# Optimization experiments

Measured on AMD Instinct MI355X. Metric: run time of the kernel, lower is better.

The kernel has to match this reference:

```python
import jax, jax.numpy as jnp
import numpy as np

B, S, D, H, DF = 8, 1024, 1024, 16, 4096
DK = D // H
EPS = 1e-5


def setup_inputs() -> dict:
    key = jax.random.key(0)
    ks = jax.random.split(key, 16)
    w = lambda k, shape: (jax.random.normal(k, shape, jnp.float32) * 0.02)
    inp = {
        "x": jax.random.normal(ks[0], (B, S, D), jnp.float32),
        "mask": jnp.ones((B, 1, 1, S), jnp.int32),
        # attention projections (torch Linear: y = x @ W.T + b)
        "Wq": w(ks[1], (D, D)), "bq": jnp.zeros((D,), jnp.float32),
        "Wk": w(ks[2], (D, D)), "bk": jnp.zeros((D,), jnp.float32),
        "Wv": w(ks[3], (D, D)), "bv": jnp.zeros((D,), jnp.float32),
        "Wo": w(ks[4], (D, D)), "bo": jnp.zeros((D,), jnp.float32),
        "ln_attn_g": jnp.ones((D,), jnp.float32), "ln_attn_b": jnp.zeros((D,), jnp.float32),
        # feed-forward
        "W1": w(ks[5], (DF, D)), "b1": jnp.zeros((DF,), jnp.float32),
        "W2": w(ks[6], (D, DF)), "b2": jnp.zeros((D,), jnp.float32),
        "ln_ff_g": jnp.ones((D,), jnp.float32), "ln_ff_b": jnp.zeros((D,), jnp.float32),
        # BatchNorm1d(d_ff) inside FFN (eval mode: running stats)
        "bnff_g": jnp.ones((DF,), jnp.float32), "bnff_b": jnp.zeros((DF,), jnp.float32),
        "bnff_m": jnp.zeros((DF,), jnp.float32), "bnff_v": jnp.ones((DF,), jnp.float32),
        # BatchNorm1d(d_model) after each sublayer (eval mode)
        "bn1_g": jnp.ones((D,), jnp.float32), "bn1_b": jnp.zeros((D,), jnp.float32),
        "bn1_m": jnp.zeros((D,), jnp.float32), "bn1_v": jnp.ones((D,), jnp.float32),
        "bn2_g": jnp.ones((D,), jnp.float32), "bn2_b": jnp.zeros((D,), jnp.float32),
        "bn2_m": jnp.zeros((D,), jnp.float32), "bn2_v": jnp.ones((D,), jnp.float32),
    }
    return inp


def _layernorm(x, g, b):
    mu = jnp.mean(x, axis=-1, keepdims=True)
    var = jnp.mean(jnp.square(x - mu), axis=-1, keepdims=True)
    return (x - mu) * jax.lax.rsqrt(var + EPS) * g + b


def _batchnorm_eval(x, g, b, m, v):
    # x: [B,S,C]; BatchNorm1d over channel C (the transpose->bn->transpose in torch
    # is equivalent to per-channel affine normalization on the last dim in eval mode)
    return (x - m) * jax.lax.rsqrt(v + EPS) * g + b


def reference(x, mask, Wq, bq, Wk, bk, Wv, bv, Wo, bo, ln_attn_g, ln_attn_b,
              W1, b1, W2, b2, ln_ff_g, ln_ff_b,
              bnff_g, bnff_b, bnff_m, bnff_v,
              bn1_g, bn1_b, bn1_m, bn1_v,
              bn2_g, bn2_b, bn2_m, bn2_v):
    # ---- Multi-head self-attention (pre-LN on query/key/value input) ----
    xq = _layernorm(x, ln_attn_g, ln_attn_b)
    q = (xq @ Wq.T + bq).reshape(B, S, H, DK)
    k = (x @ Wk.T + bk).reshape(B, S, H, DK)   # note: original applies LN only to `query`;
    v = (x @ Wv.T + bv).reshape(B, S, H, DK)   # key/value are passed raw (same x here)
    scores = jnp.einsum("bqhd,bkhd->bhqk", q, k) / np.sqrt(DK).astype(np.float32)
    scores = jnp.where(mask == 0, jnp.float32(-1e9), scores)
    attn = jax.nn.softmax(scores, axis=-1)                      # [B,H,S,S]
    context = jnp.einsum("bhqk,bkhd->bqhd", attn, v).reshape(B, S, D)
    attn_out = context @ Wo.T + bo
    x = x + attn_out                                            # residual (eval: no dropout)
    x = _batchnorm_eval(x, bn1_g, bn1_b, bn1_m, bn1_v)
    # ---- Position-wise FFN ----
    xn = _layernorm(x, ln_ff_g, ln_ff_b)
    h = jax.nn.gelu(xn @ W1.T + b1, approximate=False)          # [B,S,DF]
    h = _batchnorm_eval(h, bnff_g, bnff_b, bnff_m, bnff_v)
    ff = h @ W2.T + b2
    x = x + ff
    x = _batchnorm_eval(x, bn2_g, bn2_b, bn2_m, bn2_v)
    return x, attn
```

## Files before the change

kernel.cpp:

```cpp
#include <hip/hip_runtime.h>
#include <hip/hip_bf16.h>
#include <math.h>

typedef __hip_bfloat16 bf16;
typedef __attribute__((ext_vector_type(8))) short short8;
typedef __attribute__((ext_vector_type(4))) short short4v;
typedef __attribute__((ext_vector_type(4))) float f32x4;

#define DEV static __device__ __forceinline__

DEV short f2bf(float f) {
    bf16 h = __float2bfloat16(f);
    return __builtin_bit_cast(short, h);
}

DEV void glds16(const void* g, void* l) {
    __builtin_amdgcn_global_load_lds((const __attribute__((address_space(1))) void*)g,
                                     (__attribute__((address_space(3))) void*)l, 16, 0, 0);
}

__global__ __launch_bounds__(256) void cast_all(const float* __restrict__ Wq,
                                                const float* __restrict__ Wk,
                                                const float* __restrict__ Wv,
                                                const float* __restrict__ Wo,
                                                const float* __restrict__ W1,
                                                const float* __restrict__ W2,
                                                bf16* __restrict__ wqkv, bf16* __restrict__ wo,
                                                bf16* __restrict__ w1, bf16* __restrict__ w2) {
    int i = blockIdx.x * 256 + threadIdx.x;
    const float* src;
    bf16* dst;
    int si, di;
    if (i < 786432) {
        src = (i < 262144) ? Wq : (i < 524288) ? Wk : Wv;
        si = (i < 262144) ? i : (i < 524288) ? i - 262144 : i - 524288;
        dst = wqkv; di = i;
    } else if (i < 1048576) {
        src = Wo; si = i - 786432; dst = wo; di = si;
    } else if (i < 2097152) {
        src = W1; si = i - 1048576; dst = w1; di = si;
    } else {
        src = W2; si = i - 2097152; dst = w2; di = si;
    }
    f32x4 v = ((const f32x4*)src)[si];
    short4v o;
    #pragma unroll
    for (int j = 0; j < 4; j++) o[j] = f2bf(v[j]);
    ((short4v*)dst)[di] = o;
}

__global__ __launch_bounds__(256) void affine_all(
    const float* __restrict__ g1, const float* __restrict__ bb1, const float* __restrict__ m1, const float* __restrict__ v1,
    const float* __restrict__ g2, const float* __restrict__ bb2, const float* __restrict__ m2, const float* __restrict__ v2,
    const float* __restrict__ gf, const float* __restrict__ bbf, const float* __restrict__ mf, const float* __restrict__ vf,
    float* __restrict__ s1, float* __restrict__ t1, float* __restrict__ s2, float* __restrict__ t2,
    float* __restrict__ sf, float* __restrict__ tf) {
    int i = blockIdx.x * 256 + threadIdx.x;
    const float *g, *b, *m, *v; float *s, *t; int j;
    if (i < 1024)      { g = g1; b = bb1; m = m1; v = v1; s = s1; t = t1; j = i; }
    else if (i < 2048) { g = g2; b = bb2; m = m2; v = v2; s = s2; t = t2; j = i - 1024; }
    else               { g = gf; b = bbf; m = mf; v = vf; s = sf; t = tf; j = i - 2048; }
    float sc = g[j] * rsqrtf(v[j] + 1e-5f);
    s[j] = sc;
    t[j] = b[j] - m[j] * sc;
}

__global__ __launch_bounds__(256) void ln_kernel(const float* __restrict__ x,
                                                 const float* __restrict__ g,
                                                 const float* __restrict__ b,
                                                 bf16* __restrict__ lnout,
                                                 bf16* __restrict__ rawout) {
    const int row = blockIdx.x, t = threadIdx.x;
    const float* xr = x + (size_t)row * 1024;
    f32x4 v = ((const f32x4*)xr)[t];
    float s = v[0] + v[1] + v[2] + v[3];
    float sq = v[0]*v[0] + v[1]*v[1] + v[2]*v[2] + v[3]*v[3];
    #pragma unroll
    for (int off = 1; off < 64; off <<= 1) {
        s  += __shfl_xor(s, off);
        sq += __shfl_xor(sq, off);
    }
    __shared__ float ls[4], lq[4];
    if ((t & 63) == 0) { ls[t >> 6] = s; lq[t >> 6] = sq; }
    __syncthreads();
    s = ls[0] + ls[1] + ls[2] + ls[3];
    sq = lq[0] + lq[1] + lq[2] + lq[3];
    float mu = s * (1.0f / 1024.0f);
    float rs = rsqrtf(sq * (1.0f / 1024.0f) - mu * mu + 1e-5f);
    f32x4 gg = ((const f32x4*)g)[t];
    f32x4 bb = ((const f32x4*)b)[t];
    short4v o;
    #pragma unroll
    for (int j = 0; j < 4; j++) o[j] = f2bf((v[j] - mu) * rs * gg[j] + bb[j]);
    ((short4v*)(lnout + (size_t)row * 1024))[t] = o;
    if (rawout) {
        short4v r;
        #pragma unroll
        for (int j = 0; j < 4; j++) r[j] = f2bf(v[j]);
        ((short4v*)(rawout + (size_t)row * 1024))[t] = r;
    }
}

enum { M_RESBN = 0, M_GELU = 1, M_QKV = 2 };

template <int BN, int MODE>
__global__ __launch_bounds__(512, 2) void gemm8(
    const bf16* __restrict__ A0, const bf16* __restrict__ A1, const bf16* __restrict__ Bw,
    const float* __restrict__ b0, const float* __restrict__ b1, const float* __restrict__ b2,
    void* __restrict__ o0, void* __restrict__ o1, void* __restrict__ o2,
    const float* __restrict__ res, const float* __restrict__ sa, const float* __restrict__ ta,
    int N, int K) {
    constexpr int NB = BN / 64;
    constexpr int SB = BN * 128;
    constexpr int CW = BN / 4;
    constexpr int NF = CW / 16;
    __shared__ char smem[65536 + 2 * SB];

    const int tid = threadIdx.x, lane = tid & 63, wid = tid >> 6;
    const int gx = gridDim.x;
    const int n_wg = gx * gridDim.y;
    int lin = blockIdx.y * gx + blockIdx.x;
    lin = (lin & 7) * (n_wg >> 3) + (lin >> 3);
    const int bn = (lin % gx) * BN, bm = (lin / gx) << 8;

    const int wr = wid >> 2, wc = wid & 3;
    const int arow = lane & 15, hi = lane >> 4;
    const int xr = arow & 7;
    const int ck0 = (hi ^ xr) << 3;
    const int ck1 = ((4 + hi) ^ xr) << 3;
    const int rowA = wr * 128 + arow;
    const int rowB = wc * CW + arow;

    const bf16* Asel;
    if constexpr (MODE == M_QKV) Asel = (bn < 1024) ? A0 : A1;
    else                         Asel = A0;

    const int rS = tid >> 3;
    const int cXor = ((tid & 7) ^ (rS & 7)) << 3;
    const bf16* gA = Asel + (size_t)(bm + rS) * K + cXor;
    const bf16* gB = Bw   + (size_t)(bn + rS) * K + cXor;

    f32x4 acc[8][NF] = {};

    auto stA = [&](int t, int i) {
        glds16(gA + (size_t)i * 64 * K + t * 64,
               smem + ((t & 1) << 15) + i * 8192 + (wid << 10));
    };
    auto stB = [&](int t, int i) {
        glds16(gB + (size_t)i * 64 * K + t * 64,
               smem + 65536 + (t & 1) * SB + i * 8192 + (wid << 10));
    };

    const int NT = K >> 6;
    #pragma unroll
    for (int i = 0; i < NB; i++) stB(0, i);
    stA(0, 0); stA(0, 2); stA(0, 1); stA(0, 3);

#define PHASE(Q)                                                                              \
    do {                                                                                      \
        const short8 a00 = *(const short8*)(Ap + (rowA + (2*(Q)) * 16) * 64 + ck0);           \
        const short8 a01 = *(const short8*)(Ap + (rowA + (2*(Q)) * 16) * 64 + ck1);           \
        const short8 a10 = *(const short8*)(Ap + (rowA + (2*(Q)+1) * 16) * 64 + ck0);         \
        const short8 a11 = *(const short8*)(Ap + (rowA + (2*(Q)+1) * 16) * 64 + ck1);         \
        __builtin_amdgcn_s_setprio(1);                                                        \
        _Pragma("unroll")                                                                     \
        for (int n = 0; n < NF; n++) {                                                        \
            acc[2*(Q)][n]   = __builtin_amdgcn_mfma_f32_16x16x32_bf16(a00, bva[n], acc[2*(Q)][n], 0, 0, 0);   \
            acc[2*(Q)][n]   = __builtin_amdgcn_mfma_f32_16x16x32_bf16(a01, bvb[n], acc[2*(Q)][n], 0, 0, 0);   \
            acc[2*(Q)+1][n] = __builtin_amdgcn_mfma_f32_16x16x32_bf16(a10, bva[n], acc[2*(Q)+1][n], 0, 0, 0); \
            acc[2*(Q)+1][n] = __builtin_amdgcn_mfma_f32_16x16x32_bf16(a11, bvb[n], acc[2*(Q)+1][n], 0, 0, 0); \
        }                                                                                     \
        __builtin_amdgcn_s_setprio(0);                                                        \
    } while (0)

    for (int t = 0; t < NT; ++t) {
        const int p = t & 1;
        const bf16* Ap = (const bf16*)(smem + (p << 15));
        const bf16* Bp = (const bf16*)(smem + 65536 + p * SB);
        asm volatile("s_waitcnt vmcnt(2)" ::: "memory");
        __builtin_amdgcn_s_barrier();
        if (t + 1 < NT) {
            stB(t + 1, 0);
            if constexpr (NB == 4) stB(t + 1, 1);
        }
        short8 bva[NF], bvb[NF];
        #pragma unroll
        for (int n = 0; n < NF; n++) {
            bva[n] = *(const short8*)(Bp + (rowB + n * 16) * 64 + ck0);
            bvb[n] = *(const short8*)(Bp + (rowB + n * 16) * 64 + ck1);
        }
        PHASE(0);
        __builtin_amdgcn_s_barrier();
        if (t + 1 < NT) {
            if constexpr (NB == 4) { stB(t + 1, 2); stB(t + 1, 3); }
            else                   { stB(t + 1, 1); }
        }
        PHASE(1);
        if (t == NT - 1) asm volatile("s_waitcnt vmcnt(0)" ::: "memory");
        else if constexpr (NB == 4) asm volatile("s_waitcnt vmcnt(4)" ::: "memory");
        else                        asm volatile("s_waitcnt vmcnt(2)" ::: "memory");
        __builtin_amdgcn_s_barrier();
        if (t + 1 < NT) { stA(t + 1, 0); stA(t + 1, 2); }
        PHASE(2);
        __builtin_amdgcn_s_barrier();
        if (t + 1 < NT) { stA(t + 1, 1); stA(t + 1, 3); }
        PHASE(3);
    }
#undef PHASE

    #pragma unroll
    for (int mf = 0; mf < 8; mf++) {
        #pragma unroll
        for (int nf = 0; nf < NF; nf++) {
            const int col = bn + wc * CW + nf * 16 + arow;
            #pragma unroll
            for (int j = 0; j < 4; j++) {
                const int row = bm + wr * 128 + mf * 16 + hi * 4 + j;
                if constexpr (MODE == M_RESBN) {
                    float v = acc[mf][nf][j] + b0[col];
                    size_t idx = (size_t)row * N + col;
                    ((float*)o0)[idx] = (res[idx] + v) * sa[col] + ta[col];
                } else if constexpr (MODE == M_GELU) {
                    float v = acc[mf][nf][j] + b0[col];
                    float ge = 0.5f * v * (1.0f + erff(v * 0.70710678118f));
                    ((bf16*)o0)[(size_t)row * N + col] = __float2bfloat16(ge * sa[col] + ta[col]);
                } else {
                    const int reg = col >> 10, c = col & 1023;
                    const float bb = (reg == 0) ? b0[c] : (reg == 1) ? b1[c] : b2[c];
                    float v = acc[mf][nf][j] + bb;
                    if (reg == 0)
                        ((bf16*)o0)[(size_t)row * 1024 + c] = __float2bfloat16(v * 0.125f);
                    else if (reg == 1)
                        ((bf16*)o1)[(size_t)row * 1024 + c] = __float2bfloat16(v);
                    else
                        ((bf16*)o2)[((size_t)(row >> 10) << 20) + ((size_t)c << 10) + (row & 1023)] =
                            __float2bfloat16(v);
                }
            }
        }
    }
}

__global__ __launch_bounds__(256) void fattn_kernel(const bf16* __restrict__ q,
                                                    const bf16* __restrict__ k,
                                                    const bf16* __restrict__ vT,
                                                    const int* __restrict__ mask,
                                                    float* __restrict__ attn,
                                                    bf16* __restrict__ ctx) {
    const int bh = blockIdx.y, b = bh >> 4, h = bh & 15;
    const int q0 = blockIdx.x << 5;
    const int tid = threadIdx.x, lane = tid & 63, wid = tid >> 6;
    const int cb = wid << 8;
    const int arow = lane & 15, hi = lane >> 4, koff = hi << 3;
    const int rbase = hi << 2;

    __shared__ char smem[65536];
    float* red = (float*)smem;

    short8 qf[2];
    #pragma unroll
    for (int m = 0; m < 2; m++)
        qf[m] = *(const short8*)(q + ((size_t)((b << 10) + q0 + (m << 4) + arow) << 10) + (h << 6) + koff);

    f32x4 acc[2][16];
    #pragma unroll
    for (int m = 0; m < 2; m++)
        #pragma unroll
        for (int n = 0; n < 16; n++) acc[m][n] = (f32x4){0.f, 0.f, 0.f, 0.f};

    #pragma unroll
    for (int n = 0; n < 16; n++) {
        short8 kf = *(const short8*)(k + ((size_t)((b << 10) + cb + (n << 4) + arow) << 10) + (h << 6) + koff);
        acc[0][n] = __builtin_amdgcn_mfma_f32_16x16x32_bf16(qf[0], kf, acc[0][n], 0, 0, 0);
        acc[1][n] = __builtin_amdgcn_mfma_f32_16x16x32_bf16(qf[1], kf, acc[1][n], 0, 0, 0);
    }

    float rmax[2][4];
    #pragma unroll
    for (int m = 0; m < 2; m++)
        #pragma unroll
        for (int j = 0; j < 4; j++) rmax[m][j] = -3.0e38f;

    #pragma unroll
    for (int n = 0; n < 16; n++) {
        const float madd = mask[(b << 10) + cb + (n << 4) + arow] ? 0.0f : -1e9f;
        #pragma unroll
        for (int m = 0; m < 2; m++)
            #pragma unroll
            for (int j = 0; j < 4; j++) {
                acc[m][n][j] += madd;
                rmax[m][j] = fmaxf(rmax[m][j], acc[m][n][j]);
            }
    }
    #pragma unroll
    for (int off = 1; off < 16; off <<= 1)
        #pragma unroll
        for (int m = 0; m < 2; m++)
            #pragma unroll
            for (int j = 0; j < 4; j++) rmax[m][j] = fmaxf(rmax[m][j], __shfl_xor(rmax[m][j], off));

    if ((lane & 15) == 0) {
        #pragma unroll
        for (int m = 0; m < 2; m++)
            #pragma unroll
            for (int j = 0; j < 4; j++) red[(wid << 5) + (m << 4) + rbase + j] = rmax[m][j];
    }
    __syncthreads();
    #pragma unroll
    for (int m = 0; m < 2; m++)
        #pragma unroll
        for (int j = 0; j < 4; j++) {
            int r = (m << 4) + rbase + j;
            rmax[m][j] = fmaxf(fmaxf(red[r], red[32 + r]), fmaxf(red[64 + r], red[96 + r]));
        }

    float rsum[2][4] = {};
    #pragma unroll
    for (int n = 0; n < 16; n++)
        #pragma unroll
        for (int m = 0; m < 2; m++)
            #pragma unroll
            for (int j = 0; j < 4; j++) {
                float p = __expf(acc[m][n][j] - rmax[m][j]);
                acc[m][n][j] = p;
                rsum[m][j] += p;
            }
    #pragma unroll
    for (int off = 1; off < 16; off <<= 1)
        #pragma unroll
        for (int m = 0; m < 2; m++)
            #pragma unroll
            for (int j = 0; j < 4; j++) rsum[m][j] += __shfl_xor(rsum[m][j], off);

    if ((lane & 15) == 0) {
        #pragma unroll
        for (int m = 0; m < 2; m++)
            #pragma unroll
            for (int j = 0; j < 4; j++) red[128 + (wid << 5) + (m << 4) + rbase + j] = rsum[m][j];
    }
    __syncthreads();
    float inv[2][4];
    #pragma unroll
    for (int m = 0; m < 2; m++)
        #pragma unroll
        for (int j = 0; j < 4; j++) {
            int r = 128 + (m << 4) + rbase + j;
            inv[m][j] = 1.0f / (red[r] + red[32 + r] + red[64 + r] + red[96 + r]);
        }
    __syncthreads();

    char* ptw = smem + (wid << 14);
    const size_t obase = (((size_t)bh << 10) + q0) << 10;
    #pragma unroll
    for (int m = 0; m < 2; m++)
        #pragma unroll
        for (int j = 0; j < 4; j++) {
            const int qr = (m << 4) + rbase + j;
            float* orow = attn + obase + ((size_t)qr << 10) + cb;
            const float iv = inv[m][j];
            #pragma unroll
            for (int n = 0; n < 16; n++) {
                float p = acc[m][n][j] * iv;
                orow[(n << 4) + arow] = p;
                const int col = (n << 4) + arow;
                *(bf16*)(ptw + (qr << 9) + ((col << 1) ^ ((qr & 7) << 4))) = __float2bfloat16(p);
            }
        }

    f32x4 acc2[2][4];
    #pragma unroll
    for (int m = 0; m < 2; m++)
        #pragma unroll
        for (int n = 0; n < 4; n++) acc2[m][n] = (f32x4){0.f, 0.f, 0.f, 0.f};

    #pragma unroll
    for (int kk = 0; kk < 8; kk++) {
        short8 af[2];
        #pragma unroll
        for (int m = 0; m < 2; m++)
            af[m] = *(const short8*)(ptw + (((m << 4) + arow) << 9) +
                                     (((kk << 6) + (hi << 4)) ^ ((arow & 7) << 4)));
        #pragma unroll
        for (int n = 0; n < 4; n++) {
            short8 vf = *(const short8*)(vT + ((size_t)((b << 10) + (h << 6) + (n << 4) + arow) << 10) +
                                         cb + (kk << 5) + koff);
            acc2[0][n] = __builtin_amdgcn_mfma_f32_16x16x32_bf16(af[0], vf, acc2[0][n], 0, 0, 0);
            acc2[1][n] = __builtin_amdgcn_mfma_f32_16x16x32_bf16(af[1], vf, acc2[1][n], 0, 0, 0);
        }
    }

    __syncthreads();
    float* part = (float*)smem;
    #pragma unroll
    for (int m = 0; m < 2; m++)
        #pragma unroll
        for (int n = 0; n < 4; n++)
            #pragma unroll
            for (int j = 0; j < 4; j++)
                part[wid * 2304 + ((m << 4) + rbase + j) * 72 + (n << 4) + arow] = acc2[m][n][j];
    __syncthreads();

    const int qrow = tid >> 3, dkb = (tid & 7) << 3;
    f32x4 sa = (f32x4){0.f, 0.f, 0.f, 0.f}, sb = (f32x4){0.f, 0.f, 0.f, 0.f};
    #pragma unroll
    for (int w = 0; w < 4; w++) {
        const float* p = part + w * 2304 + qrow * 72 + dkb;
        f32x4 a = *(const f32x4*)p;
        f32x4 c = *(const f32x4*)(p + 4);
        sa[0] += a[0]; sa[1] += a[1]; sa[2] += a[2]; sa[3] += a[3];
        sb[0] += c[0]; sb[1] += c[1]; sb[2] += c[2]; sb[3] += c[3];
    }
    short8 o;
    o[0] = f2bf(sa[0]); o[1] = f2bf(sa[1]); o[2] = f2bf(sa[2]); o[3] = f2bf(sa[3]);
    o[4] = f2bf(sb[0]); o[5] = f2bf(sb[1]); o[6] = f2bf(sb[2]); o[7] = f2bf(sb[3]);
    *(short8*)(ctx + ((size_t)((b << 10) + q0 + qrow) << 10) + (h << 6) + dkb) = o;
}

extern "C" void kernel_launch(void* const* d_in, const int* in_sizes, int n_in,
                              void* d_out, int out_size, void* d_ws, size_t ws_size,
                              hipStream_t stream) {
    (void)in_sizes; (void)n_in; (void)out_size; (void)ws_size;
    const float* x   = (const float*)d_in[0];
    const int*   mask= (const int*)d_in[1];
    const float* Wq  = (const float*)d_in[2];  const float* bq  = (const float*)d_in[3];
    const float* Wk  = (const float*)d_in[4];  const float* bk  = (const float*)d_in[5];
    const float* Wv  = (const float*)d_in[6];  const float* bv  = (const float*)d_in[7];
    const float* Wo  = (const float*)d_in[8];  const float* bo  = (const float*)d_in[9];
    const float* lag = (const float*)d_in[10]; const float* lab = (const float*)d_in[11];
    const float* W1  = (const float*)d_in[12]; const float* b1  = (const float*)d_in[13];
    const float* W2  = (const float*)d_in[14]; const float* b2  = (const float*)d_in[15];
    const float* lfg = (const float*)d_in[16]; const float* lfb = (const float*)d_in[17];
    const float* bffg= (const float*)d_in[18]; const float* bffb= (const float*)d_in[19];
    const float* bffm= (const float*)d_in[20]; const float* bffv= (const float*)d_in[21];
    const float* b1g = (const float*)d_in[22]; const float* b1b = (const float*)d_in[23];
    const float* b1m = (const float*)d_in[24]; const float* b1v = (const float*)d_in[25];
    const float* b2g = (const float*)d_in[26]; const float* b2b = (const float*)d_in[27];
    const float* b2m = (const float*)d_in[28]; const float* b2v = (const float*)d_in[29];

    char* ws = (char*)d_ws;
    const size_t MB = 1024 * 1024;
    bf16* wqkv_bf = (bf16*)(ws);
    bf16* wo_bf   = (bf16*)(ws + 6 * MB);
    bf16* w1_bf   = (bf16*)(ws + 8 * MB);
    bf16* w2_bf   = (bf16*)(ws + 16 * MB);
    float* s1  = (float*)(ws + 24 * MB); float* t1  = s1 + 1024;
    float* s2  = t1 + 1024;              float* t2  = s2 + 1024;
    float* sff = t2 + 1024;              float* tff = sff + 4096;
    bf16* x_bf   = (bf16*)(ws + 25 * MB);
    bf16* xq_bf  = (bf16*)(ws + 41 * MB);
    bf16* q_bf   = (bf16*)(ws + 57 * MB);
    bf16* k_bf   = (bf16*)(ws + 73 * MB);
    bf16* vT_bf  = (bf16*)(ws + 89 * MB);
    bf16* ctx_bf = (bf16*)(ws + 105 * MB);
    float* x1    = (float*)(ws + 121 * MB);
    bf16* xn_bf  = (bf16*)(ws + 153 * MB);
    bf16* h_bf   = (bf16*)(ws + 169 * MB);

    float* out_x    = (float*)d_out;
    float* out_attn = out_x + (size_t)8 * 1024 * 1024;

    cast_all<<<12288, 256, 0, stream>>>(Wq, Wk, Wv, Wo, W1, W2, wqkv_bf, wo_bf, w1_bf, w2_bf);
    affine_all<<<24, 256, 0, stream>>>(b1g, b1b, b1m, b1v, b2g, b2b, b2m, b2v,
                                       bffg, bffb, bffm, bffv, s1, t1, s2, t2, sff, tff);

    ln_kernel<<<8192, 256, 0, stream>>>(x, lag, lab, xq_bf, x_bf);

    gemm8<128, M_QKV><<<dim3(24, 32), 512, 0, stream>>>(
        xq_bf, x_bf, wqkv_bf, bq, bk, bv, q_bf, k_bf, vT_bf, nullptr, nullptr, nullptr, 1024, 1024);

    fattn_kernel<<<dim3(32, 128), 256, 0, stream>>>(q_bf, k_bf, vT_bf, mask, out_attn, ctx_bf);

    gemm8<128, M_RESBN><<<dim3(8, 32), 512, 0, stream>>>(
        ctx_bf, nullptr, wo_bf, bo, nullptr, nullptr, x1, nullptr, nullptr, x, s1, t1, 1024, 1024);

    ln_kernel<<<8192, 256, 0, stream>>>(x1, lfg, lfb, xn_bf, nullptr);
    gemm8<256, M_GELU><<<dim3(16, 32), 512, 0, stream>>>(
        xn_bf, nullptr, w1_bf, b1, nullptr, nullptr, h_bf, nullptr, nullptr, nullptr, sff, tff, 4096, 1024);
    gemm8<128, M_RESBN><<<dim3(8, 32), 512, 0, stream>>>(
        h_bf, nullptr, w2_bf, b2, nullptr, nullptr, out_x, nullptr, nullptr, x1, s2, t2, 1024, 4096);
}
```

Baseline: 664.8 us.

## Add two-phase pipelined 128x256 GEMM and fix attention QK head-dim coverage

Adds a new gemm2p kernel that uses 128x256 tiles with double-buffered direct-to-LDS loads. It splits each K-step into two phases with separate barriers, so the next B and A tile loads overlap with the MFMA work. It also raises MFMA wave priority and targets two workgroups per CU. The kernel replaces the QKV, output-projection and FFN-down GEMMs. The attention kernel now also multiplies the second half of the 64-wide head dimension; previously only 32 of the 64 elements entered the QK^T scores. That correction adds MFMA work and loads to attention, and the larger GEMM tile may reduce the number of workgroups available to fill the GPU.

New measurement: 698.2 us. +5.0%, slower.

```diff
diff --git a/kernel.cpp b/kernel.cpp
--- a/kernel.cpp
+++ b/kernel.cpp
@@ -241,6 +241,126 @@
     }
 }
 
+template <int MODE>
+__global__ __launch_bounds__(512, 2) void gemm2p(
+    const bf16* __restrict__ A0, const bf16* __restrict__ A1, const bf16* __restrict__ Bw,
+    const float* __restrict__ b0, const float* __restrict__ b1, const float* __restrict__ b2,
+    void* __restrict__ o0, void* __restrict__ o1, void* __restrict__ o2,
+    const float* __restrict__ res, const float* __restrict__ sa, const float* __restrict__ ta,
+    int N, int K) {
+    __shared__ char smem[98304];
+
+    const int tid = threadIdx.x, lane = tid & 63, wid = tid >> 6;
+    const int gx = gridDim.x;
+    const int n_wg = gx * gridDim.y;
+    int lin = blockIdx.y * gx + blockIdx.x;
+    lin = (lin & 7) * (n_wg >> 3) + (lin >> 3);
+    const int bn = (lin % gx) << 8, bm = (lin / gx) << 7;
+
+    const int wr = wid >> 2, wc = wid & 3;
+    const int arow = lane & 15, hi = lane >> 4;
+    const int xr = arow & 7;
+    const int ck0 = (hi ^ xr) << 3;
+    const int ck1 = ((4 + hi) ^ xr) << 3;
+    const int rowB = wc * 64 + arow;
+
+    const bf16* Asel;
+    if constexpr (MODE == M_QKV) Asel = (bn < 1024) ? A0 : A1;
+    else                         Asel = A0;
+
+    const int rS = tid >> 3;
+    const int cXor = ((tid & 7) ^ (rS & 7)) << 3;
+    const int gRowA = (rS & 31) + ((rS >> 5) << 6);
+    const bf16* gA = Asel + (size_t)(bm + gRowA) * K + cXor;
+    const bf16* gB = Bw + (size_t)(bn + rS) * K + cXor;
+
+    f32x4 acc[4][4] = {};
+
+    auto stA = [&](int t, int i) {
+        glds16(gA + (size_t)i * 32 * K + t * 64,
+               smem + ((t & 1) << 14) + i * 8192 + (wid << 10));
+    };
+    auto stB = [&](int t, int i) {
+        glds16(gB + (size_t)i * 64 * K + t * 64,
+               smem + 32768 + ((t & 1) << 15) + i * 8192 + (wid << 10));
+    };
+
+    const int NT = K >> 6;
+    stB(0, 0); stB(0, 1); stB(0, 2); stB(0, 3);
+    stA(0, 0); stA(0, 1);
+
+#define AROW(MF) (((MF) & 1) * 16 + ((MF) >> 1) * 64 + wr * 32 + arow)
+#define MFSTEP(MF)                                                                            \
+    do {                                                                                      \
+        const short8 a0 = *(const short8*)(Ap + AROW(MF) * 64 + ck0);                         \
+        const short8 a1 = *(const short8*)(Ap + AROW(MF) * 64 + ck1);                         \
+        __builtin_amdgcn_s_setprio(1);                                                        \
+        _Pragma("unroll")                                                                     \
+        for (int n = 0; n < 4; n++) {                                                         \
+            acc[MF][n] = __builtin_amdgcn_mfma_f32_16x16x32_bf16(a0, bva[n], acc[MF][n], 0, 0, 0); \
+            acc[MF][n] = __builtin_amdgcn_mfma_f32_16x16x32_bf16(a1, bvb[n], acc[MF][n], 0, 0, 0); \
+        }                                                                                     \
+        __builtin_amdgcn_s_setprio(0);                                                        \
+    } while (0)
+
+    for (int t = 0; t < NT; ++t) {
+        const int p = t & 1;
+        const bf16* Ap = (const bf16*)(smem + (p << 14));
+        const bf16* Bp = (const bf16*)(smem + 32768 + (p << 15));
+        asm volatile("s_waitcnt vmcnt(1)" ::: "memory");
+        __builtin_amdgcn_s_barrier();
+        if (t + 1 < NT) { stB(t + 1, 0); stB(t + 1, 1); stB(t + 1, 2); stB(t + 1, 3); }
+        short8 bva[4], bvb[4];
+        #pragma unroll
+        for (int n = 0; n < 4; n++) {
+            bva[n] = *(const short8*)(Bp + (rowB + n * 16) * 64 + ck0);
+            bvb[n] = *(const short8*)(Bp + (rowB + n * 16) * 64 + ck1);
+        }
+        MFSTEP(0);
+        MFSTEP(1);
+        if (t == NT - 1) asm volatile("s_waitcnt vmcnt(0)" ::: "memory");
+        else             asm volatile("s_waitcnt vmcnt(4)" ::: "memory");
+        __builtin_amdgcn_s_barrier();
+        if (t + 1 < NT) { stA(t + 1, 0); stA(t + 1, 1); }
+        MFSTEP(2);
+        MFSTEP(3);
+    }
+#undef MFSTEP
+#undef AROW
+
+    #pragma unroll
+    for (int mf = 0; mf < 4; mf++) {
+        #pragma unroll
+        for (int nf = 0; nf < 4; nf++) {
+            const int col = bn + wc * 64 + nf * 16 + arow;
+            #pragma unroll
+            for (int j = 0; j < 4; j++) {
+                const int row = bm + wr * 64 + mf * 16 + hi * 4 + j;
+                if constexpr (MODE == M_RESBN) {
+                    float v = acc[mf][nf][j] + b0[col];
+                    size_t idx = (size_t)row * N + col;
+                    ((float*)o0)[idx] = (res[idx] + v) * sa[col] + ta[col];
+                } else if constexpr (MODE == M_GELU) {
+                    float v = acc[mf][nf][j] + b0[col];
+                    float ge = 0.5f * v * (1.0f + erff(v * 0.70710678118f));
+                    ((bf16*)o0)[(size_t)row * N + col] = __float2bfloat16(ge * sa[col] + ta[col]);
+                } else {
+                    const int reg = col >> 10, c = col & 1023;
+                    const float bb = (reg == 0) ? b0[c] : (reg == 1) ? b1[c] : b2[c];
+                    float v = acc[mf][nf][j] + bb;
+                    if (reg == 0)
+                        ((bf16*)o0)[(size_t)row * 1024 + c] = __float2bfloat16(v * 0.125f);
+                    else if (reg == 1)
+                        ((bf16*)o1)[(size_t)row * 1024 + c] = __float2bfloat16(v);
+                    else
+                        ((bf16*)o2)[((size_t)(row >> 10) << 20) + ((size_t)c << 10) + (row & 1023)] =
+                            __float2bfloat16(v);
+                }
+            }
+        }
+    }
+}
+
 __global__ __launch_bounds__(256) void fattn_kernel(const bf16* __restrict__ q,
                                                     const bf16* __restrict__ k,
                                                     const bf16* __restrict__ vT,
@@ -257,22 +377,29 @@
     __shared__ char smem[65536];
     float* red = (float*)smem;
 
-    short8 qf[2];
+    short8 qf[2], qf2[2];
+    #pragma unroll
+    for (int m = 0; m < 2; m++) {
+        const bf16* qp = q + ((size_t)((b << 10) + q0 + (m << 4) + arow) << 10) + (h << 6);
+        qf[m]  = *(const short8*)(qp + koff);
+        qf2[m] = *(const short8*)(qp + 32 + koff);
+    }
+
+    f32x4 acc[2][16];
     #pragma unroll
     for (int m = 0; m < 2; m++)
-        qf[m] = *(const short8*)(q + ((size_t)((b << 10) + q0 + (m << 4) + arow) << 10) + (h << 6) + koff);
-
-    f32x4 acc[2][16];
-    #pragma unroll
-    for (int m = 0; m < 2; m++)
         #pragma unroll
         for (int n = 0; n < 16; n++) acc[m][n] = (f32x4){0.f, 0.f, 0.f, 0.f};
 
     #pragma unroll
     for (int n = 0; n < 16; n++) {
-        short8 kf = *(const short8*)(k + ((size_t)((b << 10) + cb + (n << 4) + arow) << 10) + (h << 6) + koff);
-        acc[0][n] = __builtin_amdgcn_mfma_f32_16x16x32_bf16(qf[0], kf, acc[0][n], 0, 0, 0);
-        acc[1][n] = __builtin_amdgcn_mfma_f32_16x16x32_bf16(qf[1], kf, acc[1][n], 0, 0, 0);
+        const bf16* kp = k + ((size_t)((b << 10) + cb + (n << 4) + arow) << 10) + (h << 6);
+        short8 kf  = *(const short8*)(kp + koff);
+        short8 kf2 = *(const short8*)(kp + 32 + koff);
+        acc[0][n] = __builtin_amdgcn_mfma_f32_16x16x32_bf16(qf[0],  kf,  acc[0][n], 0, 0, 0);
+        acc[0][n] = __builtin_amdgcn_mfma_f32_16x16x32_bf16(qf2[0], kf2, acc[0][n], 0, 0, 0);
+        acc[1][n] = __builtin_amdgcn_mfma_f32_16x16x32_bf16(qf[1],  kf,  acc[1][n], 0, 0, 0);
+        acc[1][n] = __builtin_amdgcn_mfma_f32_16x16x32_bf16(qf2[1], kf2, acc[1][n], 0, 0, 0);
     }
 
     float rmax[2][4];
@@ -465,17 +592,17 @@
 
     ln_kernel<<<8192, 256, 0, stream>>>(x, lag, lab, xq_bf, x_bf);
 
-    gemm8<128, M_QKV><<<dim3(24, 32), 512, 0, stream>>>(
+    gemm2p<M_QKV><<<dim3(12, 64), 512, 0, stream>>>(
         xq_bf, x_bf, wqkv_bf, bq, bk, bv, q_bf, k_bf, vT_bf, nullptr, nullptr, nullptr, 1024, 1024);
 
     fattn_kernel<<<dim3(32, 128), 256, 0, stream>>>(q_bf, k_bf, vT_bf, mask, out_attn, ctx_bf);
 
-    gemm8<128, M_RESBN><<<dim3(8, 32), 512, 0, stream>>>(
+    gemm2p<M_RESBN><<<dim3(4, 64), 512, 0, stream>>>(
         ctx_bf, nullptr, wo_bf, bo, nullptr, nullptr, x1, nullptr, nullptr, x, s1, t1, 1024, 1024);
 
     ln_kernel<<<8192, 256, 0, stream>>>(x1, lfg, lfb, xn_bf, nullptr);
     gemm8<256, M_GELU><<<dim3(16, 32), 512, 0, stream>>>(
         xn_bf, nullptr, w1_bf, b1, nullptr, nullptr, h_bf, nullptr, nullptr, nullptr, sff, tff, 4096, 1024);
-    gemm8<128, M_RESBN><<<dim3(8, 32), 512, 0, stream>>>(
+    gemm2p<M_RESBN><<<dim3(4, 64), 512, 0, stream>>>(
         h_bf, nullptr, w2_bf, b2, nullptr, nullptr, out_x, nullptr, nullptr, x1, s2, t2, 1024, 4096);
 }
```
